# Kernel optimization log

Measured on AMD Instinct MI355X. Metric: run time of the kernel, lower is better.

## Reference

```python
import jax, jax.numpy as jnp
import numpy as np

D = 1024       # nn_embed
I = 512        # ffn_intermediate_size
E = 7          # num routed experts (8 total - 1 shared)
TOPK = 2
B, S = 4, 4096


def setup_inputs() -> dict:
    key = jax.random.key(0)
    ks = jax.random.split(key, 10)
    s = 0.02
    return {
        "x": jax.random.normal(ks[0], (B, S, D), dtype=jnp.float32),
        # shared expert (one): weights stored so y = x @ W
        "sh_gate": jax.random.normal(ks[1], (D, I), dtype=jnp.float32) * s,
        "sh_up":   jax.random.normal(ks[2], (D, I), dtype=jnp.float32) * s,
        "sh_down": jax.random.normal(ks[3], (I, D), dtype=jnp.float32) * s,
        # routed experts stacked [E, ...]
        "r_gate": jax.random.normal(ks[4], (E, D, I), dtype=jnp.float32) * s,
        "r_up":   jax.random.normal(ks[5], (E, D, I), dtype=jnp.float32) * s,
        "r_down": jax.random.normal(ks[6], (E, I, D), dtype=jnp.float32) * s,
        # router linear (has bias in torch) + learnable routing_bias param
        "w_r": jax.random.normal(ks[7], (D, E), dtype=jnp.float32) * s,
        "b_r": jnp.zeros((E,), dtype=jnp.float32),
        "routing_bias": jnp.zeros((E,), dtype=jnp.float32),
    }


def _expert(xt, wg, wu, wd):
    # SwiGLU: down(silu(gate(x)) * up(x))
    return (jax.nn.silu(xt @ wg) * (xt @ wu)) @ wd


def reference(x, sh_gate, sh_up, sh_down, r_gate, r_up, r_down, w_r, b_r, routing_bias):
    Bx, Sx, Dx = x.shape
    T = Bx * Sx
    xt = x.reshape(T, Dx)

    # shared expert (num_shared_experts == 1, no averaging)
    shared_out = _expert(xt, sh_gate, sh_up, sh_down)

    # sigmoid routing with top-k and renormalized combine weights
    logits = xt @ w_r + b_r + routing_bias          # [T, E]
    probs = jax.nn.sigmoid(logits)
    top_p, top_i = jax.lax.top_k(probs, TOPK)       # [T, k]
    top_p = top_p / jnp.sum(top_p, axis=-1, keepdims=True)

    # dense combine-weight matrix: zero where expert not selected
    comb = jnp.zeros((T, E), dtype=x.dtype).at[
        jnp.arange(T)[:, None], top_i].add(top_p)   # [T, E]

    routed_out = jnp.zeros_like(xt)
    for e in range(E):  # small fixed expert count
        y = _expert(xt, r_gate[e], r_up[e], r_down[e])
        routed_out = routed_out + y * comb[:, e:e + 1]

    return (shared_out + routed_out).reshape(Bx, Sx, Dx)
```

## Files before the change

### kernel.cpp

```cpp
#include <hip/hip_runtime.h>
#include <hip/hip_bf16.h>
#include <cstdint>
#include <cstddef>

#define DTOK 1024
#define IFF  512
#define NEXP 7
#define TTOK 16384
#define CAP  (2*TTOK + NEXP*256)
#define CAPX (CAP + TTOK)

typedef __bf16 v8bf  __attribute__((ext_vector_type(8)));
typedef float  f32x4 __attribute__((ext_vector_type(4)));

#define AS1 __attribute__((address_space(1)))
#define AS3 __attribute__((address_space(3)))


__global__ void init_kernel(int* __restrict__ slot_token, float* __restrict__ slot_w,
                            __bf16* __restrict__ zpage) {
    int i = blockIdx.x * 256 + threadIdx.x;
    if (i < CAP) slot_token[i] = -1;
    else if (i < CAPX) { slot_token[i] = i - CAP; slot_w[i] = 1.f; }
    if (i < 2048) zpage[i] = (__bf16)0.f;
}

__global__ void cast_x_kernel(const float4* __restrict__ x, __bf16* __restrict__ xb) {
    int i = blockIdx.x * 256 + threadIdx.x;
    float4 v = x[i];
    typedef __bf16 v4bf __attribute__((ext_vector_type(4)));
    v4bf o; o[0] = (__bf16)v.x; o[1] = (__bf16)v.y; o[2] = (__bf16)v.z; o[3] = (__bf16)v.w;
    *reinterpret_cast<v4bf*>(xb + (size_t)i * 4) = o;
}

__global__ __launch_bounds__(256) void build_B1t(
    const float* __restrict__ r_gate, const float* __restrict__ r_up,
    const float* __restrict__ sh_gate, const float* __restrict__ sh_up,
    __bf16* __restrict__ B1) {
    const int kh = blockIdx.x, j = blockIdx.y, e = blockIdx.z;
    const float* G = (e < NEXP) ? (r_gate + (size_t)e * (DTOK * IFF)) : sh_gate;
    const float* U = (e < NEXP) ? (r_up   + (size_t)e * (DTOK * IFF)) : sh_up;
    __shared__ __bf16 lg[16][520];
    __shared__ __bf16 lu[16][520];
    const int tid = threadIdx.x;
    const int c4 = tid & 3, kk0 = tid >> 2;
    #pragma unroll
    for (int p = 0; p < 8; ++p) {
        int kk = kk0 + p * 64;
        size_t off = (size_t)(kh * 512 + kk) * IFF + j * 16 + c4 * 4;
        float4 g = *(const float4*)&G[off];
        float4 u = *(const float4*)&U[off];
        lg[c4*4+0][kk] = (__bf16)g.x; lg[c4*4+1][kk] = (__bf16)g.y;
        lg[c4*4+2][kk] = (__bf16)g.z; lg[c4*4+3][kk] = (__bf16)g.w;
        lu[c4*4+0][kk] = (__bf16)u.x; lu[c4*4+1][kk] = (__bf16)u.y;
        lu[c4*4+2][kk] = (__bf16)u.z; lu[c4*4+3][kk] = (__bf16)u.w;
    }
    __syncthreads();
    const int rr = tid >> 3;
    const int ch0 = tid & 7;
    const int cc = rr & 15;
    const bool isup = rr >= 16;
    const int r = j * 32 + (isup ? 16 : 0) + cc;
    const __bf16* src = isup ? &lu[cc][0] : &lg[cc][0];
    __bf16* dst = B1 + ((size_t)e << 20) + (size_t)r * DTOK + kh * 512;
    #pragma unroll
    for (int q = 0; q < 8; ++q) {
        int ch = ch0 + q * 8;
        *(v8bf*)&dst[ch * 8] = *(const v8bf*)&src[ch * 8];
    }
}

__global__ __launch_bounds__(256) void build_B2t(
    const float* __restrict__ r_down, const float* __restrict__ sh_down,
    __bf16* __restrict__ B2) {
    const int kh = blockIdx.x, nb = blockIdx.y, e = blockIdx.z;
    const float* D = (e < NEXP) ? (r_down + (size_t)e * (IFF * DTOK)) : sh_down;
    __shared__ __bf16 ln[64][264];
    const int tid = threadIdx.x;
    const int c4 = tid & 15, kk0 = tid >> 4;
    #pragma unroll
    for (int p = 0; p < 16; ++p) {
        int kk = kk0 + p * 16;
        size_t off = (size_t)(kh * 256 + kk) * DTOK + nb * 64 + c4 * 4;
        float4 v = *(const float4*)&D[off];
        ln[c4*4+0][kk] = (__bf16)v.x; ln[c4*4+1][kk] = (__bf16)v.y;
        ln[c4*4+2][kk] = (__bf16)v.z; ln[c4*4+3][kk] = (__bf16)v.w;
    }
    __syncthreads();
    const int nn = tid >> 2;
    const int ch0 = tid & 3;
    __bf16* dst = B2 + ((size_t)e * 1024 + nb * 64 + nn) * IFF + kh * 256;
    #pragma unroll
    for (int q = 0; q < 8; ++q) {
        int ch = ch0 + q * 4;
        *(v8bf*)&dst[ch * 8] = *(const v8bf*)&ln[nn][ch * 8];
    }
}

__global__ __launch_bounds__(256) void router_kernel(
    const float* __restrict__ x, const float* __restrict__ w_r,
    const float* __restrict__ b_r, const float* __restrict__ rb,
    int* __restrict__ top_i, float* __restrict__ top_w) {
    int wid = threadIdx.x >> 6, lane = threadIdx.x & 63;
    int t = blockIdx.x * 4 + wid;
    float acc[NEXP] = {0.f,0.f,0.f,0.f,0.f,0.f,0.f};
    #pragma unroll 4
    for (int it = 0; it < DTOK / 64; ++it) {
        int d = it * 64 + lane;
        float xv = x[(size_t)t * DTOK + d];
        const float* wr = w_r + (size_t)d * NEXP;
        #pragma unroll
        for (int e = 0; e < NEXP; ++e) acc[e] += xv * wr[e];
    }
    #pragma unroll
    for (int e = 0; e < NEXP; ++e)
        #pragma unroll
        for (int off = 32; off; off >>= 1) acc[e] += __shfl_xor(acc[e], off);
    if (lane == 0) {
        float p[NEXP];
        #pragma unroll
        for (int e = 0; e < NEXP; ++e) p[e] = 1.f / (1.f + expf(-(acc[e] + b_r[e] + rb[e])));
        int i0 = 0;
        #pragma unroll
        for (int e = 1; e < NEXP; ++e) if (p[e] > p[i0]) i0 = e;
        int i1 = -1;
        #pragma unroll
        for (int e = 0; e < NEXP; ++e) if (e != i0 && (i1 < 0 || p[e] > p[i1])) i1 = e;
        float s = p[i0] + p[i1];
        top_i[2 * t] = i0; top_i[2 * t + 1] = i1;
        top_w[2 * t] = p[i0] / s; top_w[2 * t + 1] = p[i1] / s;
    }
}

__global__ __launch_bounds__(1024) void gather_kernel(
    const int* __restrict__ top_i, const float* __restrict__ top_w,
    int* __restrict__ slot_token, float* __restrict__ slot_w,
    int* __restrict__ tok_slot, int* __restrict__ offs_out) {
    __shared__ int h[NEXP][1024];
    __shared__ int lofs[NEXP];
    const int tid = threadIdx.x;
    const int base = tid * 32;

    int cnt[NEXP] = {0,0,0,0,0,0,0};
    int emem[32];
    float wmem[32];
    #pragma unroll
    for (int j = 0; j < 32; ++j) {
        emem[j] = top_i[base + j];
        wmem[j] = top_w[base + j];
        #pragma unroll
        for (int q = 0; q < NEXP; ++q) if (emem[j] == q) cnt[q]++;
    }
    #pragma unroll
    for (int q = 0; q < NEXP; ++q) h[q][tid] = cnt[q];
    __syncthreads();
    for (int off = 1; off < 1024; off <<= 1) {
        int v[NEXP];
        #pragma unroll
        for (int q = 0; q < NEXP; ++q) v[q] = (tid >= off) ? h[q][tid - off] : 0;
        __syncthreads();
        #pragma unroll
        for (int q = 0; q < NEXP; ++q) h[q][tid] += v[q];
        __syncthreads();
    }
    if (tid == 0) {
        int o = 0;
        #pragma unroll
        for (int q = 0; q < NEXP; ++q) { lofs[q] = o; o += ((h[q][1023] + 255) >> 8) << 8; }
        #pragma unroll
        for (int q = 0; q < NEXP; ++q) offs_out[q] = lofs[q];
        offs_out[NEXP] = CAP;
    }
    __syncthreads();
    int pos[NEXP];
    #pragma unroll
    for (int q = 0; q < NEXP; ++q) pos[q] = lofs[q] + h[q][tid] - cnt[q];
    #pragma unroll
    for (int j = 0; j < 32; ++j) {
        int t = (base + j) >> 1;
        #pragma unroll
        for (int q = 0; q < NEXP; ++q) if (emem[j] == q) {
            slot_token[pos[q]] = t;
            slot_w[pos[q]] = wmem[j];
            tok_slot[base + j] = pos[q];
            pos[q]++;
        }
    }
}


#define BARX()  asm volatile("s_barrier" ::: "memory")
#define LGKM0() do { asm volatile("s_waitcnt lgkmcnt(0)" ::: "memory"); \
                     __builtin_amdgcn_sched_barrier(0); } while (0)
#define VMW(n)  do { asm volatile("s_waitcnt vmcnt(" #n ")" ::: "memory"); \
                     __builtin_amdgcn_sched_barrier(0); } while (0)

#define MMQ(mh, nh)                                                            \
  do {                                                                         \
    __builtin_amdgcn_sched_barrier(0);                                         \
    __builtin_amdgcn_s_setprio(1);                                             \
    _Pragma("unroll")                                                          \
    for (int mi = 0; mi < 4; ++mi)                                             \
      _Pragma("unroll")                                                        \
      for (int nj = 0; nj < 2; ++nj)                                           \
        _Pragma("unroll")                                                      \
        for (int ks = 0; ks < 2; ++ks)                                         \
          acc[(mh)*4+mi][(nh)*2+nj] = __builtin_amdgcn_mfma_f32_16x16x32_bf16( \
              afr[(mh)*4+mi][ks], bfr[nj][ks],                                 \
              acc[(mh)*4+mi][(nh)*2+nj], 0, 0, 0);                             \
    __builtin_amdgcn_s_setprio(0);                                             \
    __builtin_amdgcn_sched_barrier(0);                                         \
  } while (0)

#define READ_A(mh)                                                             \
  do {                                                                         \
    _Pragma("unroll")                                                          \
    for (int mi = 0; mi < 4; ++mi) {                                           \
      afr[(mh)*4+mi][0] = *(const v8bf*)&As[ab + ((mh)*4+mi)*1024 + kko0];     \
      afr[(mh)*4+mi][1] = *(const v8bf*)&As[ab + ((mh)*4+mi)*1024 + kko1];     \
    }                                                                          \
  } while (0)

#define READ_B(nh)                                                             \
  do {                                                                         \
    _Pragma("unroll")                                                          \
    for (int nj = 0; nj < 2; ++nj) {                                           \
      bfr[nj][0] = *(const v8bf*)&Bs[bb + ((nh)*2+nj)*1024 + kko0];            \
      bfr[nj][1] = *(const v8bf*)&Bs[bb + ((nh)*2+nj)*1024 + kko1];            \
    }                                                                          \
  } while (0)

#define STAGE_A(tau, h)                                                        \
  do {                                                                         \
    const int _b = (tau) & 1;                                                  \
    __builtin_amdgcn_global_load_lds((const AS1 void*)(aptr[h][0] + (tau)*64), \
        (AS3 void*)&As[(_b*2 + (h))*8192 + tid*8], 16, 0, 0);                  \
    __builtin_amdgcn_global_load_lds((const AS1 void*)(aptr[h][1] + (tau)*64), \
        (AS3 void*)&As[(_b*2 + (h))*8192 + 4096 + tid*8], 16, 0, 0);           \
  } while (0)

#define STAGE_B(tau, h)                                                        \
  do {                                                                         \
    const int _b = (tau) & 1;                                                  \
    __builtin_amdgcn_global_load_lds((const AS1 void*)(bptr[h][0] + (tau)*64), \
        (AS3 void*)&Bs[(_b*2 + (h))*8192 + tid*8], 16, 0, 0);                  \
    __builtin_amdgcn_global_load_lds((const AS1 void*)(bptr[h][1] + (tau)*64), \
        (AS3 void*)&Bs[(_b*2 + (h))*8192 + 4096 + tid*8], 16, 0, 0);           \
  } while (0)

template<int KDIM, int EPI, bool GATHER, typename YT>
__global__ __launch_bounds__(512, 2) void gemm8_kernel(
    const __bf16* __restrict__ A, const __bf16* __restrict__ Bmat,
    const int* __restrict__ offs, const int* __restrict__ slot_token,
    const float* __restrict__ slot_w, const int* __restrict__ tok_slot,
    YT* __restrict__ yr,
    __bf16* __restrict__ Hout, float* __restrict__ out,
    const __bf16* __restrict__ zpage) {
    constexpr int NKT = KDIM / 64;
    const int nwg = gridDim.x;
    const int q8 = nwg >> 3, r8 = nwg & 7;
    const int xcd = blockIdx.x & 7, jj = blockIdx.x >> 3;
    const int L = (xcd < r8 ? xcd * (q8 + 1) : r8 * (q8 + 1) + (xcd - r8) * q8) + jj;
    const int tileN = L & 3;
    const int tileM = L >> 2;
    const int tid = threadIdx.x, lane = tid & 63, wid = tid >> 6;
    const int wm = wid >> 2, wn = wid & 3;

    __shared__ __bf16 As[2 * 2 * 8192];
    __shared__ __bf16 Bs[2 * 2 * 8192];

    const __bf16* Bp = Bmat;
    if (offs) {
        int m0 = tileM * 256, e = 0;
        #pragma unroll
        for (int i = 1; i < NEXP + 1; ++i) if (m0 >= offs[i]) e = i;
        Bp = Bmat + (size_t)e * (1024 * KDIM);
    }

    const __bf16* aptr[2][2];
    const __bf16* bptr[2][2];
    #pragma unroll
    for (int h = 0; h < 2; ++h)
        #pragma unroll
        for (int l = 0; l < 2; ++l) {
            const int i = tid + l * 512;
            const int rh = i >> 3;
            const int swzo = (((tid & 7) ^ (rh & 7)) << 3);
            const int ra = tileM * 256 + h * 128 + rh;
            if (GATHER) {
                int tok = slot_token[ra];
                aptr[h][l] = (tok >= 0 ? A + (size_t)tok * KDIM : zpage) + swzo;
            } else {
                aptr[h][l] = A + (size_t)ra * KDIM + swzo;
            }
            const int rbg = tileN * 256 + h * 128 + rh;
            bptr[h][l] = Bp + (size_t)rbg * KDIM + swzo;
        }

    const int kko0 = (((lane >> 4) ^ (lane & 7)) << 3);
    const int kko1 = (((4 + (lane >> 4)) ^ (lane & 7)) << 3);
    const int arow = (lane & 15) * 64;

    f32x4 acc[8][4] = {};
    v8bf afr[8][2];
    v8bf bfr[2][2];

    STAGE_B(0, 0); STAGE_B(0, 1); STAGE_A(0, 0); STAGE_A(0, 1);
    STAGE_A(1, 0); STAGE_B(1, 0); STAGE_B(1, 1);
    VMW(6);
    BARX();

    #pragma unroll 2
    for (int t = 0; t < NKT; ++t) {
        const int ab = ((t & 1) * 2 + wm) * 8192 + arow;
        const int bb = ((t & 1) * 2 + (wn >> 1)) * 8192 + (wn & 1) * 4096 + arow;
        READ_A(0);
        READ_B(0);
        if (t + 1 < NKT) STAGE_A(t + 1, 1);
        BARX();
        LGKM0();
        MMQ(0, 0);
        BARX();
        READ_A(1);
        BARX();
        LGKM0();
        MMQ(1, 0);
        BARX();
        READ_B(1);
        if (t + 2 < NKT) STAGE_A(t + 2, 0);
        BARX();
        LGKM0();
        MMQ(0, 1);
        BARX();
        if (t + 2 < NKT) {
            STAGE_B(t + 2, 0);
            STAGE_B(t + 2, 1);
            VMW(6);
        } else if (t + 1 < NKT) {
            VMW(0);
        }
        BARX();
        MMQ(1, 1);
        BARX();
    }

    const int mbase = tileM * 256 + wm * 128;
    const int nbase = tileN * 256 + wn * 64;
    const int rowoff = (lane >> 4) * 4;
    const int col = lane & 15;

    if constexpr (EPI == 0) {
        #pragma unroll
        for (int mi = 0; mi < 8; ++mi)
            #pragma unroll
            for (int pi = 0; pi < 2; ++pi) {
                int ni = pi * 2;
                int hcol = (((nbase + ni * 16) >> 5) << 4) + col;
                #pragma unroll
                for (int j = 0; j < 4; ++j) {
                    int m = mbase + mi * 16 + rowoff + j;
                    float g = acc[mi][ni][j];
                    float u = acc[mi][ni + 1][j];
                    float h = (g / (1.f + __expf(-g))) * u;
                    Hout[(size_t)m * IFF + hcol] = (__bf16)h;
                }
            }
    } else if constexpr (EPI == 1) {
        #pragma unroll
        for (int mi = 0; mi < 8; ++mi)
            #pragma unroll
            for (int j = 0; j < 4; ++j) {
                int m = mbase + mi * 16 + rowoff + j;
                #pragma unroll
                for (int ni = 0; ni < 4; ++ni)
                    out[(size_t)m * DTOK + nbase + ni * 16 + col] = acc[mi][ni][j];
            }
    } else if constexpr (EPI == 2) {
        #pragma unroll
        for (int mi = 0; mi < 8; ++mi)
            #pragma unroll
            for (int j = 0; j < 4; ++j) {
                int m = mbase + mi * 16 + rowoff + j;
                if (slot_token[m] < 0) continue;
                float wgt = slot_w[m];
                #pragma unroll
                for (int ni = 0; ni < 4; ++ni)
                    yr[(size_t)m * DTOK + nbase + ni * 16 + col] = (YT)(wgt * acc[mi][ni][j]);
            }
    } else if constexpr (EPI == 3) {
        #pragma unroll
        for (int mi = 0; mi < 8; ++mi)
            #pragma unroll
            for (int j = 0; j < 4; ++j) {
                int m = mbase + mi * 16 + rowoff + j;
                int s0 = tok_slot[2 * m], s1 = tok_slot[2 * m + 1];
                const YT* y0 = yr + (size_t)s0 * DTOK;
                const YT* y1 = yr + (size_t)s1 * DTOK;
                #pragma unroll
                for (int ni = 0; ni < 4; ++ni) {
                    int c = nbase + ni * 16 + col;
                    out[(size_t)m * DTOK + c] = acc[mi][ni][j] + (float)y0[c] + (float)y1[c];
                }
            }
    } else {
        #pragma unroll
        for (int mi = 0; mi < 8; ++mi)
            #pragma unroll
            for (int j = 0; j < 4; ++j) {
                int m = mbase + mi * 16 + rowoff + j;
                int tok = slot_token[m];
                if (tok < 0) continue;
                float wgt = slot_w[m];
                #pragma unroll
                for (int ni = 0; ni < 4; ++ni)
                    atomicAdd(out + (size_t)tok * DTOK + nbase + ni * 16 + col, wgt * acc[mi][ni][j]);
            }
    }
}

extern "C" void kernel_launch(void* const* d_in, const int* in_sizes, int n_in,
                              void* d_out, int out_size, void* d_ws, size_t ws_size,
                              hipStream_t stream) {
    const float* x       = (const float*)d_in[0];
    const float* sh_gate = (const float*)d_in[1];
    const float* sh_up   = (const float*)d_in[2];
    const float* sh_down = (const float*)d_in[3];
    const float* r_gate  = (const float*)d_in[4];
    const float* r_up    = (const float*)d_in[5];
    const float* r_down  = (const float*)d_in[6];
    const float* w_r     = (const float*)d_in[7];
    const float* b_r     = (const float*)d_in[8];
    const float* rb      = (const float*)d_in[9];
    float* out = (float*)d_out;

    char* w = (char*)d_ws;
    __bf16* xb = (__bf16*)w;          w += (size_t)TTOK * DTOK * 2;
    __bf16* B1 = (__bf16*)w;          w += (size_t)8 * 1024 * 1024 * 2;
    __bf16* B2 = (__bf16*)w;          w += (size_t)8 * 1024 * 512 * 2;
    __bf16* H  = (__bf16*)w;          w += (size_t)CAPX * IFF * 2;
    int*    top_i = (int*)w;          w += (size_t)TTOK * 2 * 4;
    float*  top_w = (float*)w;        w += (size_t)TTOK * 2 * 4;
    int*    slot_token = (int*)w;     w += (size_t)CAPX * 4;
    float*  slot_w = (float*)w;       w += (size_t)CAPX * 4;
    int*    tok_slot = (int*)w;       w += (size_t)TTOK * 2 * 4;
    int*    offs = (int*)w;           w += 256;
    __bf16* zpage = (__bf16*)w;       w += 4096;
    void*   Yr = (void*)w;
    size_t used = (size_t)(w - (char*)d_ws);
    size_t rem = (ws_size > used) ? (ws_size - used) : 0;
    bool have_yr = rem >= (size_t)CAP * DTOK * 2;

    init_kernel<<<(CAPX + 255) / 256, 256, 0, stream>>>(slot_token, slot_w, zpage);
    cast_x_kernel<<<(TTOK * DTOK / 4) / 256, 256, 0, stream>>>((const float4*)x, xb);
    build_B1t<<<dim3(2, 32, 8), 256, 0, stream>>>(r_gate, r_up, sh_gate, sh_up, B1);
    build_B2t<<<dim3(2, 16, 8), 256, 0, stream>>>(r_down, sh_down, B2);
    router_kernel<<<TTOK / 4, 256, 0, stream>>>(x, w_r, b_r, rb, top_i, top_w);
    gather_kernel<<<1, 1024, 0, stream>>>(top_i, top_w, slot_token, slot_w, tok_slot, offs);

    dim3 blk(512);
    gemm8_kernel<DTOK, 0, true, __bf16><<<(CAPX / 256) * 4, blk, 0, stream>>>(
        xb, B1, offs, slot_token, nullptr, nullptr, nullptr, H, nullptr, zpage);

    if (have_yr) {
        __bf16* yr = (__bf16*)Yr;
        gemm8_kernel<IFF, 2, false, __bf16><<<(CAP / 256) * 4, blk, 0, stream>>>(
            H, B2, offs, slot_token, slot_w, nullptr, yr, nullptr, nullptr, zpage);
        gemm8_kernel<IFF, 3, false, __bf16><<<(TTOK / 256) * 4, blk, 0, stream>>>(
            H + (size_t)CAP * IFF, B2 + (size_t)NEXP * 1024 * 512,
            nullptr, nullptr, nullptr, tok_slot, yr, nullptr, out, zpage);
    } else {
        gemm8_kernel<IFF, 1, false, __bf16><<<(TTOK / 256) * 4, blk, 0, stream>>>(
            H + (size_t)CAP * IFF, B2 + (size_t)NEXP * 1024 * 512,
            nullptr, nullptr, nullptr, nullptr, nullptr, nullptr, out, zpage);
        gemm8_kernel<IFF, 4, false, __bf16><<<(CAP / 256) * 4, blk, 0, stream>>>(
            H, B2, offs, slot_token, slot_w, nullptr, nullptr, nullptr, out, zpage);
    }
}
```

Before: 408.5 us.

## Software-pipeline LDS fragment reads across K tiles and use 32-bit offsets

Restructures the GEMM main loop so the first A/B fragment reads for the next K tile are issued during the last MFMA quarter of the current tile. A second B-fragment register set lets reads overlap compute, and barriers per tile drop from seven to four. The last two iterations are peeled with compile-time flags instead of runtime branches. Per-thread 64-bit global pointers become 32-bit offsets, and the expert index goes through readfirstlane, to cut VGPR and address cost. The zero page is removed: padded gather rows now load token 0, so padding rows of H hold non-zero data and the code relies on those slots never being read back.

```diff
diff --git a/kernel.cpp b/kernel.cpp
--- a/kernel.cpp
+++ b/kernel.cpp
@@ -17,12 +17,10 @@
 #define AS3 __attribute__((address_space(3)))
 
 
-__global__ void init_kernel(int* __restrict__ slot_token, float* __restrict__ slot_w,
-                            __bf16* __restrict__ zpage) {
+__global__ void init_kernel(int* __restrict__ slot_token, float* __restrict__ slot_w) {
     int i = blockIdx.x * 256 + threadIdx.x;
     if (i < CAP) slot_token[i] = -1;
     else if (i < CAPX) { slot_token[i] = i - CAP; slot_w[i] = 1.f; }
-    if (i < 2048) zpage[i] = (__bf16)0.f;
 }
 
 __global__ void cast_x_kernel(const float4* __restrict__ x, __bf16* __restrict__ xb) {
@@ -195,7 +193,7 @@
 #define VMW(n)  do { asm volatile("s_waitcnt vmcnt(" #n ")" ::: "memory"); \
                      __builtin_amdgcn_sched_barrier(0); } while (0)
 
-#define MMQ(mh, nh)                                                            \
+#define MMQx(mh, nh, BF)                                                       \
   do {                                                                         \
     __builtin_amdgcn_sched_barrier(0);                                         \
     __builtin_amdgcn_s_setprio(1);                                             \
@@ -206,56 +204,93 @@
         _Pragma("unroll")                                                      \
         for (int ks = 0; ks < 2; ++ks)                                         \
           acc[(mh)*4+mi][(nh)*2+nj] = __builtin_amdgcn_mfma_f32_16x16x32_bf16( \
-              afr[(mh)*4+mi][ks], bfr[nj][ks],                                 \
+              afr[(mh)*4+mi][ks], BF[nj][ks],                                  \
               acc[(mh)*4+mi][(nh)*2+nj], 0, 0, 0);                             \
     __builtin_amdgcn_s_setprio(0);                                             \
     __builtin_amdgcn_sched_barrier(0);                                         \
   } while (0)
 
-#define READ_A(mh)                                                             \
-  do {                                                                         \
-    _Pragma("unroll")                                                          \
+#define READ_A0(AB)                                                            \
+  do { _Pragma("unroll")                                                       \
     for (int mi = 0; mi < 4; ++mi) {                                           \
-      afr[(mh)*4+mi][0] = *(const v8bf*)&As[ab + ((mh)*4+mi)*1024 + kko0];     \
-      afr[(mh)*4+mi][1] = *(const v8bf*)&As[ab + ((mh)*4+mi)*1024 + kko1];     \
-    }                                                                          \
-  } while (0)
-
-#define READ_B(nh)                                                             \
-  do {                                                                         \
-    _Pragma("unroll")                                                          \
+      afr[mi][0] = *(const v8bf*)&As[(AB) + mi*1024 + kko0];                   \
+      afr[mi][1] = *(const v8bf*)&As[(AB) + mi*1024 + kko1];                   \
+    } } while (0)
+
+#define READ_A1(AB)                                                            \
+  do { _Pragma("unroll")                                                       \
+    for (int mi = 4; mi < 8; ++mi) {                                           \
+      afr[mi][0] = *(const v8bf*)&As[(AB) + mi*1024 + kko0];                   \
+      afr[mi][1] = *(const v8bf*)&As[(AB) + mi*1024 + kko1];                   \
+    } } while (0)
+
+#define READ_B0(BB)                                                            \
+  do { _Pragma("unroll")                                                       \
     for (int nj = 0; nj < 2; ++nj) {                                           \
-      bfr[nj][0] = *(const v8bf*)&Bs[bb + ((nh)*2+nj)*1024 + kko0];            \
-      bfr[nj][1] = *(const v8bf*)&Bs[bb + ((nh)*2+nj)*1024 + kko1];            \
-    }                                                                          \
-  } while (0)
+      bfr0[nj][0] = *(const v8bf*)&Bs[(BB) + nj*1024 + kko0];                  \
+      bfr0[nj][1] = *(const v8bf*)&Bs[(BB) + nj*1024 + kko1];                  \
+    } } while (0)
+
+#define READ_B1(BB)                                                            \
+  do { _Pragma("unroll")                                                       \
+    for (int nj = 0; nj < 2; ++nj) {                                           \
+      bfr1[nj][0] = *(const v8bf*)&Bs[(BB) + (2+nj)*1024 + kko0];              \
+      bfr1[nj][1] = *(const v8bf*)&Bs[(BB) + (2+nj)*1024 + kko1];              \
+    } } while (0)
 
 #define STAGE_A(tau, h)                                                        \
   do {                                                                         \
     const int _b = (tau) & 1;                                                  \
-    __builtin_amdgcn_global_load_lds((const AS1 void*)(aptr[h][0] + (tau)*64), \
+    __builtin_amdgcn_global_load_lds((const AS1 void*)(Ag + aoff[h][0] + (tau)*64), \
         (AS3 void*)&As[(_b*2 + (h))*8192 + tid*8], 16, 0, 0);                  \
-    __builtin_amdgcn_global_load_lds((const AS1 void*)(aptr[h][1] + (tau)*64), \
+    __builtin_amdgcn_global_load_lds((const AS1 void*)(Ag + aoff[h][1] + (tau)*64), \
         (AS3 void*)&As[(_b*2 + (h))*8192 + 4096 + tid*8], 16, 0, 0);           \
   } while (0)
 
 #define STAGE_B(tau, h)                                                        \
   do {                                                                         \
     const int _b = (tau) & 1;                                                  \
-    __builtin_amdgcn_global_load_lds((const AS1 void*)(bptr[h][0] + (tau)*64), \
+    __builtin_amdgcn_global_load_lds((const AS1 void*)(Bp + boff[h][0] + (tau)*64), \
         (AS3 void*)&Bs[(_b*2 + (h))*8192 + tid*8], 16, 0, 0);                  \
-    __builtin_amdgcn_global_load_lds((const AS1 void*)(bptr[h][1] + (tau)*64), \
+    __builtin_amdgcn_global_load_lds((const AS1 void*)(Bp + boff[h][1] + (tau)*64), \
         (AS3 void*)&Bs[(_b*2 + (h))*8192 + 4096 + tid*8], 16, 0, 0);           \
   } while (0)
 
+#define KTILE(T, SA1, SA0, SB, WM, RN)                                         \
+  do {                                                                         \
+    const int _buf = (T) & 1;                                                  \
+    const int ab  = (_buf * 2 + wm) * 8192 + arow;                             \
+    const int bb  = (_buf * 2 + (wn >> 1)) * 8192 + (wn & 1) * 4096 + arow;    \
+    const int abn = ((1 - _buf) * 2 + wm) * 8192 + arow;                       \
+    const int bbn = ((1 - _buf) * 2 + (wn >> 1)) * 8192 + (wn & 1) * 4096 + arow; \
+    LGKM0();                                                                   \
+    MMQx(0, 0, bfr0);                                                          \
+    READ_A1(ab);                                                               \
+    if (SA1) STAGE_A((T) + 1, 1);                                              \
+    BARX();                                                                    \
+    LGKM0();                                                                   \
+    MMQx(1, 0, bfr0);                                                          \
+    READ_B1(bb);                                                               \
+    BARX();                                                                    \
+    LGKM0();                                                                   \
+    MMQx(0, 1, bfr1);                                                          \
+    if (SA0) STAGE_A((T) + 2, 0);                                              \
+    BARX();                                                                    \
+    if (SB) { STAGE_B((T) + 2, 0); STAGE_B((T) + 2, 1); }                      \
+    if (WM == 0) { VMW(6); } else if (WM == 1) { VMW(0); }                     \
+    BARX();                                                                    \
+    MMQx(1, 1, bfr1);                                                          \
+    if (RN) { READ_A0(abn); READ_B0(bbn); }                                    \
+    BARX();                                                                    \
+  } while (0)
+
 template<int KDIM, int EPI, bool GATHER, typename YT>
 __global__ __launch_bounds__(512, 2) void gemm8_kernel(
-    const __bf16* __restrict__ A, const __bf16* __restrict__ Bmat,
+    const __bf16* __restrict__ Ag, const __bf16* __restrict__ Bmat,
     const int* __restrict__ offs, const int* __restrict__ slot_token,
     const float* __restrict__ slot_w, const int* __restrict__ tok_slot,
     YT* __restrict__ yr,
-    __bf16* __restrict__ Hout, float* __restrict__ out,
-    const __bf16* __restrict__ zpage) {
+    __bf16* __restrict__ Hout, float* __restrict__ out) {
     constexpr int NKT = KDIM / 64;
     const int nwg = gridDim.x;
     const int q8 = nwg >> 3, r8 = nwg & 7;
@@ -269,16 +304,17 @@
     __shared__ __bf16 As[2 * 2 * 8192];
     __shared__ __bf16 Bs[2 * 2 * 8192];
 
-    const __bf16* Bp = Bmat;
+    int eSel = 0;
     if (offs) {
-        int m0 = tileM * 256, e = 0;
-        #pragma unroll
-        for (int i = 1; i < NEXP + 1; ++i) if (m0 >= offs[i]) e = i;
-        Bp = Bmat + (size_t)e * (1024 * KDIM);
-    }
-
-    const __bf16* aptr[2][2];
-    const __bf16* bptr[2][2];
+        int m0 = tileM * 256;
+        #pragma unroll
+        for (int i = 1; i < NEXP + 1; ++i) if (m0 >= offs[i]) eSel = i;
+        eSel = __builtin_amdgcn_readfirstlane(eSel);
+    }
+    const __bf16* Bp = Bmat + (size_t)eSel * (1024 * KDIM);
+
+    int aoff[2][2];
+    int boff[2][2];
     #pragma unroll
     for (int h = 0; h < 2; ++h)
         #pragma unroll
@@ -289,12 +325,12 @@
             const int ra = tileM * 256 + h * 128 + rh;
             if (GATHER) {
                 int tok = slot_token[ra];
-                aptr[h][l] = (tok >= 0 ? A + (size_t)tok * KDIM : zpage) + swzo;
+                aoff[h][l] = (tok >= 0 ? tok : 0) * KDIM + swzo;
             } else {
-                aptr[h][l] = A + (size_t)ra * KDIM + swzo;
+                aoff[h][l] = ra * KDIM + swzo;
             }
             const int rbg = tileN * 256 + h * 128 + rh;
-            bptr[h][l] = Bp + (size_t)rbg * KDIM + swzo;
+            boff[h][l] = rbg * KDIM + swzo;
         }
 
     const int kko0 = (((lane >> 4) ^ (lane & 7)) << 3);
@@ -303,46 +339,25 @@
 
     f32x4 acc[8][4] = {};
     v8bf afr[8][2];
-    v8bf bfr[2][2];
-
-    STAGE_B(0, 0); STAGE_B(0, 1); STAGE_A(0, 0); STAGE_A(0, 1);
+    v8bf bfr0[2][2];
+    v8bf bfr1[2][2];
+
+    STAGE_A(0, 0); STAGE_B(0, 0); STAGE_B(0, 1); STAGE_A(0, 1);
     STAGE_A(1, 0); STAGE_B(1, 0); STAGE_B(1, 1);
     VMW(6);
     BARX();
+    {
+        const int ab0 = wm * 8192 + arow;
+        const int bb0 = (wn >> 1) * 8192 + (wn & 1) * 4096 + arow;
+        READ_A0(ab0);
+        READ_B0(bb0);
+    }
 
     #pragma unroll 2
-    for (int t = 0; t < NKT; ++t) {
-        const int ab = ((t & 1) * 2 + wm) * 8192 + arow;
-        const int bb = ((t & 1) * 2 + (wn >> 1)) * 8192 + (wn & 1) * 4096 + arow;
-        READ_A(0);
-        READ_B(0);
-        if (t + 1 < NKT) STAGE_A(t + 1, 1);
-        BARX();
-        LGKM0();
-        MMQ(0, 0);
-        BARX();
-        READ_A(1);
-        BARX();
-        LGKM0();
-        MMQ(1, 0);
-        BARX();
-        READ_B(1);
-        if (t + 2 < NKT) STAGE_A(t + 2, 0);
-        BARX();
-        LGKM0();
-        MMQ(0, 1);
-        BARX();
-        if (t + 2 < NKT) {
-            STAGE_B(t + 2, 0);
-            STAGE_B(t + 2, 1);
-            VMW(6);
-        } else if (t + 1 < NKT) {
-            VMW(0);
-        }
-        BARX();
-        MMQ(1, 1);
-        BARX();
-    }
+    for (int t = 0; t < NKT - 2; ++t)
+        KTILE(t, 1, 1, 1, 0, 1);
+    KTILE(NKT - 2, 1, 0, 0, 1, 1);
+    KTILE(NKT - 1, 0, 0, 0, 2, 0);
 
     const int mbase = tileM * 256 + wm * 128;
     const int nbase = tileN * 256 + wn * 64;
@@ -444,13 +459,12 @@
     float*  slot_w = (float*)w;       w += (size_t)CAPX * 4;
     int*    tok_slot = (int*)w;       w += (size_t)TTOK * 2 * 4;
     int*    offs = (int*)w;           w += 256;
-    __bf16* zpage = (__bf16*)w;       w += 4096;
     void*   Yr = (void*)w;
     size_t used = (size_t)(w - (char*)d_ws);
     size_t rem = (ws_size > used) ? (ws_size - used) : 0;
     bool have_yr = rem >= (size_t)CAP * DTOK * 2;
 
-    init_kernel<<<(CAPX + 255) / 256, 256, 0, stream>>>(slot_token, slot_w, zpage);
+    init_kernel<<<(CAPX + 255) / 256, 256, 0, stream>>>(slot_token, slot_w);
     cast_x_kernel<<<(TTOK * DTOK / 4) / 256, 256, 0, stream>>>((const float4*)x, xb);
     build_B1t<<<dim3(2, 32, 8), 256, 0, stream>>>(r_gate, r_up, sh_gate, sh_up, B1);
     build_B2t<<<dim3(2, 16, 8), 256, 0, stream>>>(r_down, sh_down, B2);
@@ -459,20 +473,20 @@
 
     dim3 blk(512);
     gemm8_kernel<DTOK, 0, true, __bf16><<<(CAPX / 256) * 4, blk, 0, stream>>>(
-        xb, B1, offs, slot_token, nullptr, nullptr, nullptr, H, nullptr, zpage);
+        xb, B1, offs, slot_token, nullptr, nullptr, nullptr, H, nullptr);
 
     if (have_yr) {
         __bf16* yr = (__bf16*)Yr;
         gemm8_kernel<IFF, 2, false, __bf16><<<(CAP / 256) * 4, blk, 0, stream>>>(
-            H, B2, offs, slot_token, slot_w, nullptr, yr, nullptr, nullptr, zpage);
+            H, B2, offs, slot_token, slot_w, nullptr, yr, nullptr, nullptr);
         gemm8_kernel<IFF, 3, false, __bf16><<<(TTOK / 256) * 4, blk, 0, stream>>>(
             H + (size_t)CAP * IFF, B2 + (size_t)NEXP * 1024 * 512,
-            nullptr, nullptr, nullptr, tok_slot, yr, nullptr, out, zpage);
+            nullptr, nullptr, nullptr, tok_slot, yr, nullptr, out);
     } else {
         gemm8_kernel<IFF, 1, false, __bf16><<<(TTOK / 256) * 4, blk, 0, stream>>>(
             H + (size_t)CAP * IFF, B2 + (size_t)NEXP * 1024 * 512,
-            nullptr, nullptr, nullptr, nullptr, nullptr, nullptr, out, zpage);
+            nullptr, nullptr, nullptr, nullptr, nullptr, nullptr, out);
         gemm8_kernel<IFF, 4, false, __bf16><<<(CAP / 256) * 4, blk, 0, stream>>>(
-            H, B2, offs, slot_token, slot_w, nullptr, nullptr, nullptr, out, zpage);
-    }
-}
+            H, B2, offs, slot_token, slot_w, nullptr, nullptr, nullptr, out);
+    }
+}
```

New measurement: 468.8 us. +14.8%, slower.
